# Performance work log

Measured on AMD Instinct MI355X. Metric: run time of the kernel, lower is better.

The kernel has to match this reference:

```python
import jax, jax.numpy as jnp
import numpy as np

VF = 3          # vote_factor
GRID = 0.1      # grid_size
P = 4           # padded per-group capacity (stands in for data-dependent max group size)
RATIO_MAX = 5   # original drops groups needing repeat ratio > 5
EPS = 1e-5
SHIFT, BASE = 512, 1024  # 3D->1D hash (int32-safe: BASE**3 < 2**31)


def _bn_relu(x, gamma, beta):
    # BatchNorm1d in train mode over the token (batch) axis; conv input is (N, C, 1)
    m = x.mean(axis=0)
    v = jnp.mean((x - m) ** 2, axis=0)  # biased variance, as torch BN uses for normalization
    return jax.nn.relu((x - m) * jax.lax.rsqrt(v + EPS) * gamma + beta)


def _one_sample(idv, cov, ftv, W1, b1, g1, be1, W2, b2, g2, be2, W3, b3):
    N, C = ftv.shape
    V = N * VF
    # conv1x1 stack == per-token linear layers
    h = _bn_relu(ftv @ W1.T + b1, g1, be1)
    h = _bn_relu(h @ W2.T + b2, g2, be2)
    log = (h @ W3.T + b3).reshape(N, VF, 3 + C)
    off3 = log[:, :, :3]                                  # (N, VF, 3)
    coor = (cov[:, None, :] + off3).reshape(V, 3)
    grid_res = (off3 / GRID).astype(jnp.int32)            # trunc toward zero, like .int()
    ind = (idv[:, None, :] + grid_res).reshape(V, 3)
    # Degenerate inner-dict loop (tensor keys hash by identity): every vote's feature
    # offset becomes offset[n][VF-1] * 3 / VF  (len(key)==3, idx stale at VF-1)
    feat_off = log[:, VF - 1, 3:] * (3.0 / VF)            # (N, C)
    feat = jnp.broadcast_to((ftv + feat_off)[:, None, :], (N, VF, C)).reshape(V, C)

    # group votes by quantized 3D index (tuple-key dict -> hash + unique + segment ops)
    hc = jnp.clip(ind, -SHIFT, SHIFT - 1) + SHIFT
    keys = (hc[:, 0] * BASE + hc[:, 1]) * BASE + hc[:, 2]  # (V,) int32
    _, inv = jnp.unique(keys, size=V, fill_value=-1, return_inverse=True)
    inv = inv.reshape(-1)
    ones = jnp.ones((V,), jnp.int32)
    counts = jax.ops.segment_sum(ones, inv, num_segments=V)          # group sizes
    order = jnp.argsort(inv)                                          # votes sorted by group
    starts = jnp.cumsum(counts) - counts
    first = jax.ops.segment_min(jnp.arange(V, dtype=jnp.int32), inv, num_segments=V)
    first = jnp.where(counts > 0, first, 0)
    ind_buf = jnp.where((counts > 0)[:, None], ind[first], 0).astype(jnp.int32)

    cnt_safe = jnp.maximum(counts, 1)
    p = jnp.arange(P, dtype=jnp.int32)
    src_pos = starts[:, None] + (p[None, :] % cnt_safe[:, None])      # (V, P) repeat-fill
    src = order[src_pos]
    valid = (counts > 0) & (counts * RATIO_MAX >= P)                  # ceil(P/cnt) <= 5
    coor_buf = jnp.where(valid[:, None, None], coor[src], 0.0)        # (V, P, 3)
    feat_buf = jnp.where(valid[:, None, None], feat[src], 0.0)        # (V, P, C)
    return ind_buf, coor_buf, feat_buf, valid


def setup_inputs() -> dict:
    key = jax.random.key(0)
    ks = jax.random.split(key, 12)
    B, N, C = 2, 16384, 128
    s = 1.0 / np.sqrt(C)
    return {
        "ID": jax.random.randint(ks[0], (B, N, 3), 0, 100, dtype=jnp.int32),
        "CO": jax.random.normal(ks[1], (B, N, 3), jnp.float32),
        "FT": jax.random.normal(ks[2], (B, N, C), jnp.float32),
        "W1": jax.random.normal(ks[3], (C, C), jnp.float32) * s,
        "b1": jnp.zeros((C,), jnp.float32),
        "g1": 1.0 + 0.1 * jax.random.normal(ks[4], (C,), jnp.float32),
        "be1": 0.1 * jax.random.normal(ks[5], (C,), jnp.float32),
        "W2": jax.random.normal(ks[6], (C, C), jnp.float32) * s,
        "b2": jnp.zeros((C,), jnp.float32),
        "g2": 1.0 + 0.1 * jax.random.normal(ks[7], (C,), jnp.float32),
        "be2": 0.1 * jax.random.normal(ks[8], (C,), jnp.float32),
        "W3": jax.random.normal(ks[9], ((3 + C) * VF, C), jnp.float32) * s,
        "b3": 0.01 * jax.random.normal(ks[10], ((3 + C) * VF,), jnp.float32),
    }


def reference(ID, CO, FT, W1, b1, g1, be1, W2, b2, g2, be2, W3, b3):
    outs = [_one_sample(ID[i], CO[i], FT[i], W1, b1, g1, be1, W2, b2, g2, be2, W3, b3)
            for i in range(ID.shape[0])]  # small fixed batch loop
    ind_buf = jnp.stack([o[0] for o in outs])
    coor_buf = jnp.stack([o[1] for o in outs])
    feat_buf = jnp.stack([o[2] for o in outs])
    mask = jnp.stack([o[3] for o in outs])
    return ind_buf, coor_buf, feat_buf, mask
```

## Files before the change

### kernel.cpp

```cpp
#include <hip/hip_runtime.h>

constexpr int Bn = 2;
constexpr int Nn = 16384;
constexpr int Cc = 128;
constexpr int Vv = Nn * 3;
constexpr int Pp = 4;
constexpr int SB = 48;
constexpr int HB = 96;

constexpr size_t IND0  = 0;
constexpr size_t COOR0 = (size_t)Bn * Vv * 3;
constexpr size_t FEAT0 = COOR0 + (size_t)Bn * Vv * Pp * 3;
constexpr size_t MASK0 = FEAT0 + (size_t)Bn * Vv * Pp * Cc;

template<bool BNF, bool ZERO>
__global__ __launch_bounds__(256) void gemm_t(
    const float* __restrict__ A, const float* __restrict__ W,
    const float* __restrict__ bias, const float* __restrict__ part,
    const float* __restrict__ g, const float* __restrict__ be,
    float* __restrict__ out, unsigned* __restrict__ HZ)
{
    __shared__ float As[64 * 36];
    __shared__ float Ws[128 * 36];
    __shared__ float ssl[2 * Cc];

    int t = threadIdx.x;
    if constexpr (ZERO) {
        int gid = blockIdx.x * 256 + t;
        if (gid < 3 * Bn * SB * 1024 / 4)
            ((uint4*)HZ)[gid] = make_uint4(0u, 0u, 0u, 0u);
    }

    int bid = blockIdx.x;
    int s = bid >> 8, rb = bid & 255;
    const float* Ag = A + (size_t)s * Nn * Cc + (size_t)rb * 64 * Cc;
    float* outg = out + (size_t)s * Nn * Cc + (size_t)rb * 64 * Cc;

    if constexpr (BNF) {
        if (t < Cc) {
            const float* pp = part + (size_t)s * 64 * 2 * Cc;
            float sm = 0.f, sq = 0.f;
            for (int b = 0; b < 64; ++b) {
                sm += pp[(size_t)b * 2 * Cc + t];
                sq += pp[(size_t)b * 2 * Cc + Cc + t];
            }
            float m   = sm / (float)Nn;
            float var = sq / (float)Nn - m * m;
            float inv = 1.0f / sqrtf(var + 1e-5f);
            float sc  = g[t] * inv;
            ssl[t]      = sc;
            ssl[Cc + t] = be[t] - m * sc;
        }
        __syncthreads();
    }

    int tx = t & 15, ty = t >> 4;
    int arow = t >> 3, ac4 = (t & 7) * 4;
    int wrow0 = t >> 3;

    float acc[4][8];
    #pragma unroll
    for (int i = 0; i < 4; ++i)
        #pragma unroll
        for (int j = 0; j < 8; ++j) acc[i][j] = 0.f;

    float4 aR[2], wR[4];
    #pragma unroll
    for (int r = 0; r < 2; ++r)
        aR[r] = *(const float4*)(Ag + (size_t)(arow + r * 32) * Cc + ac4);
    #pragma unroll
    for (int r = 0; r < 4; ++r)
        wR[r] = *(const float4*)(W + (size_t)(wrow0 + r * 32) * Cc + ac4);

    for (int stage = 0; stage < 4; ++stage) {
        if (stage) __syncthreads();
        #pragma unroll
        for (int r = 0; r < 2; ++r) {
            float4 v = aR[r];
            if constexpr (BNF) {
                int ch = ac4;
                v.x = fmaxf(0.f, fmaf(v.x, ssl[ch + 0], ssl[Cc + ch + 0]));
                v.y = fmaxf(0.f, fmaf(v.y, ssl[ch + 1], ssl[Cc + ch + 1]));
                v.z = fmaxf(0.f, fmaf(v.z, ssl[ch + 2], ssl[Cc + ch + 2]));
                v.w = fmaxf(0.f, fmaf(v.w, ssl[ch + 3], ssl[Cc + ch + 3]));
            }
            *(float4*)&As[(arow + r * 32) * 36 + ac4] = v;
        }
        #pragma unroll
        for (int r = 0; r < 4; ++r)
            *(float4*)&Ws[(wrow0 + r * 32) * 36 + ac4] = wR[r];
        if (stage < 3) {
            int k1 = (stage + 1) * 32;
            #pragma unroll
            for (int r = 0; r < 2; ++r)
                aR[r] = *(const float4*)(Ag + (size_t)(arow + r * 32) * Cc + k1 + ac4);
            #pragma unroll
            for (int r = 0; r < 4; ++r)
                wR[r] = *(const float4*)(W + (size_t)(wrow0 + r * 32) * Cc + k1 + ac4);
        }
        __syncthreads();
        #pragma unroll
        for (int k4 = 0; k4 < 8; ++k4) {
            int k = k4 * 4;
            float4 av[4];
            #pragma unroll
            for (int i = 0; i < 4; ++i) av[i] = *(const float4*)&As[(i * 16 + ty) * 36 + k];
            #pragma unroll
            for (int j = 0; j < 8; ++j) {
                float4 wv = *(const float4*)&Ws[(j * 16 + tx) * 36 + k];
                #pragma unroll
                for (int i = 0; i < 4; ++i) {
                    float a0 = acc[i][j];
                    a0 = fmaf(av[i].x, wv.x, a0);
                    a0 = fmaf(av[i].y, wv.y, a0);
                    a0 = fmaf(av[i].z, wv.z, a0);
                    a0 = fmaf(av[i].w, wv.w, a0);
                    acc[i][j] = a0;
                }
            }
        }
    }

    #pragma unroll
    for (int j = 0; j < 8; ++j) {
        int col = j * 16 + tx;
        float bv = bias[col];
        #pragma unroll
        for (int i = 0; i < 4; ++i)
            outg[(size_t)(i * 16 + ty) * Cc + col] = acc[i][j] + bv;
    }
}


template<bool ZERO>
__global__ __launch_bounds__(256) void gemm_t2(
    const float* __restrict__ A, const float* __restrict__ W,
    const float* __restrict__ bias, const float* __restrict__ part,
    const float* __restrict__ g, const float* __restrict__ be,
    float* __restrict__ out, unsigned* __restrict__ HZ)
{
    __shared__ float As[64 * 36];
    __shared__ float Ws[128 * 36];
    __shared__ float ssl[2 * Cc];

    int t = threadIdx.x;
    if constexpr (ZERO) {
        int gid = blockIdx.x * 256 + t;
        if (gid < 3 * Bn * SB * 1024 / 4)
            ((uint4*)HZ)[gid] = make_uint4(0u, 0u, 0u, 0u);
    }

    int bid = blockIdx.x;
    int s = bid >> 8, rb = bid & 255;
    const float* Ag = A + (size_t)s * Nn * Cc + (size_t)rb * 64 * Cc;
    float* outg = out + (size_t)s * Nn * Cc + (size_t)rb * 64 * Cc;

    if (t < Cc) {
        const float* pp = part + (size_t)s * 64 * 2 * Cc;
        float sm = 0.f, sq = 0.f;
        for (int b = 0; b < 64; ++b) {
            sm += pp[(size_t)b * 2 * Cc + t];
            sq += pp[(size_t)b * 2 * Cc + Cc + t];
        }
        float m   = sm / (float)Nn;
        float var = sq / (float)Nn - m * m;
        float inv = 1.0f / sqrtf(var + 1e-5f);
        float sc  = g[t] * inv;
        ssl[t]      = sc;
        ssl[Cc + t] = be[t] - m * sc;
    }
    __syncthreads();

    int tx = t & 15, ty = t >> 4;
    int arow = t >> 3, ac4 = (t & 7) * 4;

    float acc[4][8];
    #pragma unroll
    for (int i = 0; i < 4; ++i)
        #pragma unroll
        for (int j = 0; j < 8; ++j) acc[i][j] = 0.f;

    float4 aR[2], wR[4];
    #pragma unroll
    for (int r = 0; r < 2; ++r)
        aR[r] = *(const float4*)(Ag + (size_t)(arow + r * 32) * Cc + ac4);
    #pragma unroll
    for (int r = 0; r < 4; ++r)
        wR[r] = *(const float4*)(W + (size_t)(arow + r * 32) * Cc + ac4);

    for (int stage = 0; stage < 4; ++stage) {
        int k0 = stage * 32;
        if (stage) __syncthreads();
        #pragma unroll
        for (int r = 0; r < 2; ++r) {
            float4 v = aR[r];
            int ch = k0 + ac4;
            v.x = fmaxf(0.f, fmaf(v.x, ssl[ch + 0], ssl[Cc + ch + 0]));
            v.y = fmaxf(0.f, fmaf(v.y, ssl[ch + 1], ssl[Cc + ch + 1]));
            v.z = fmaxf(0.f, fmaf(v.z, ssl[ch + 2], ssl[Cc + ch + 2]));
            v.w = fmaxf(0.f, fmaf(v.w, ssl[ch + 3], ssl[Cc + ch + 3]));
            *(float4*)&As[(arow + r * 32) * 36 + ac4] = v;
        }
        #pragma unroll
        for (int r = 0; r < 4; ++r)
            *(float4*)&Ws[(arow + r * 32) * 36 + ac4] = wR[r];
        if (stage < 3) {
            int k1 = k0 + 32;
            #pragma unroll
            for (int r = 0; r < 2; ++r)
                aR[r] = *(const float4*)(Ag + (size_t)(arow + r * 32) * Cc + k1 + ac4);
            #pragma unroll
            for (int r = 0; r < 4; ++r)
                wR[r] = *(const float4*)(W + (size_t)(arow + r * 32) * Cc + k1 + ac4);
        }
        __syncthreads();
        #pragma unroll
        for (int k4 = 0; k4 < 8; ++k4) {
            int k = k4 * 4;
            float4 av[4];
            #pragma unroll
            for (int i = 0; i < 4; ++i) av[i] = *(const float4*)&As[(i * 16 + ty) * 36 + k];
            #pragma unroll
            for (int j = 0; j < 8; ++j) {
                float4 wv = *(const float4*)&Ws[(j * 16 + tx) * 36 + k];
                #pragma unroll
                for (int i = 0; i < 4; ++i) {
                    float a0 = acc[i][j];
                    a0 = fmaf(av[i].x, wv.x, a0);
                    a0 = fmaf(av[i].y, wv.y, a0);
                    a0 = fmaf(av[i].z, wv.z, a0);
                    a0 = fmaf(av[i].w, wv.w, a0);
                    acc[i][j] = a0;
                }
            }
        }
    }
    #pragma unroll
    for (int j = 0; j < 8; ++j) {
        int col = j * 16 + tx;
        float bv = bias[col];
        #pragma unroll
        for (int i = 0; i < 4; ++i)
            outg[(size_t)(i * 16 + ty) * Cc + col] = acc[i][j] + bv;
    }
}

__global__ __launch_bounds__(256) void gemm3_fused(
    const float* __restrict__ A, const float* __restrict__ W,
    const float* __restrict__ bias, const float* __restrict__ part,
    const float* __restrict__ g, const float* __restrict__ be,
    const float* __restrict__ FT, const float* __restrict__ CO,
    const int* __restrict__ ID,
    float* __restrict__ featb, float* __restrict__ coor,
    int* __restrict__ indb, unsigned* __restrict__ keys,
    unsigned* __restrict__ idx0, unsigned* __restrict__ hist0)
{
    __shared__ float As[64 * 36];
    __shared__ float Ws[144 * 36];
    __shared__ float ssl[2 * Cc];

    int bid = blockIdx.x;
    int s = bid >> 8, rb = bid & 255;
    const float* Ag = A + (size_t)s * Nn * Cc + (size_t)rb * 64 * Cc;

    int t = threadIdx.x, tx = t & 15, ty = t >> 4;

    if (t < Cc) {
        const float* pp = part + (size_t)s * 64 * 2 * Cc;
        float sm = 0.f, sq = 0.f;
        for (int b = 0; b < 64; ++b) {
            sm += pp[(size_t)b * 2 * Cc + t];
            sq += pp[(size_t)b * 2 * Cc + Cc + t];
        }
        float m   = sm / (float)Nn;
        float var = sq / (float)Nn - m * m;
        float inv = 1.0f / sqrtf(var + 1e-5f);
        float sc  = g[t] * inv;
        ssl[t]      = sc;
        ssl[Cc + t] = be[t] - m * sc;
    }
    __syncthreads();

    float acc[4][9];
    #pragma unroll
    for (int i = 0; i < 4; ++i)
        #pragma unroll
        for (int j = 0; j < 9; ++j) acc[i][j] = 0.f;

    for (int stage = 0; stage < 4; ++stage) {
        int k0 = stage * 32;
        if (stage) __syncthreads();
        #pragma unroll
        for (int r = 0; r < 2; ++r) {
            int idx = r * 256 + t;
            int row = idx >> 3, c4 = (idx & 7) * 4;
            float4 v = *(const float4*)(Ag + (size_t)row * Cc + k0 + c4);
            int ch = k0 + c4;
            v.x = fmaxf(0.f, fmaf(v.x, ssl[ch + 0], ssl[Cc + ch + 0]));
            v.y = fmaxf(0.f, fmaf(v.y, ssl[ch + 1], ssl[Cc + ch + 1]));
            v.z = fmaxf(0.f, fmaf(v.z, ssl[ch + 2], ssl[Cc + ch + 2]));
            v.w = fmaxf(0.f, fmaf(v.w, ssl[ch + 3], ssl[Cc + ch + 3]));
            *(float4*)&As[row * 36 + c4] = v;
        }
        for (int idx = t; idx < 144 * 8; idx += 256) {
            int row = idx >> 3, c4 = (idx & 7) * 4;
            float4 v = make_float4(0.f, 0.f, 0.f, 0.f);
            if (row < 137) {
                int wr = (row < 9) ? (row / 3) * 131 + (row % 3) : row + 256;
                v = *(const float4*)(W + (size_t)wr * Cc + k0 + c4);
            }
            *(float4*)&Ws[row * 36 + c4] = v;
        }
        __syncthreads();
        #pragma unroll
        for (int k4 = 0; k4 < 8; ++k4) {
            int k = k4 * 4;
            float4 av[4];
            #pragma unroll
            for (int i = 0; i < 4; ++i) av[i] = *(const float4*)&As[(i * 16 + ty) * 36 + k];
            #pragma unroll
            for (int j = 0; j < 9; ++j) {
                float4 wv = *(const float4*)&Ws[(j * 16 + tx) * 36 + k];
                #pragma unroll
                for (int i = 0; i < 4; ++i) {
                    float a0 = acc[i][j];
                    a0 = fmaf(av[i].x, wv.x, a0);
                    a0 = fmaf(av[i].y, wv.y, a0);
                    a0 = fmaf(av[i].z, wv.z, a0);
                    a0 = fmaf(av[i].w, wv.w, a0);
                    acc[i][j] = a0;
                }
            }
        }
    }

    __syncthreads();
    __shared__ float L9[64 * 12];
    int n0 = rb * 64;
    const float* FTg = FT + ((size_t)s * Nn + n0) * Cc;
    float* FBg = featb + ((size_t)s * Nn + n0) * Cc;
    #pragma unroll
    for (int j = 0; j < 9; ++j) {
        int col = j * 16 + tx;
        if (col < 9) {
            float bv = bias[(col / 3) * 131 + col % 3];
            #pragma unroll
            for (int i = 0; i < 4; ++i)
                L9[(i * 16 + ty) * 12 + col] = acc[i][j] + bv;
        } else if (col < 137) {
            int ch = col - 9;
            float bv = bias[col + 256];
            #pragma unroll
            for (int i = 0; i < 4; ++i) {
                int row = i * 16 + ty;
                float lg = acc[i][j] + bv;
                FBg[(size_t)row * Cc + ch] = FTg[(size_t)row * Cc + ch] + lg;
            }
        }
    }
    __syncthreads();
    if (t < 192) {
        int row = t / 3, jv = t - row * 3;
        int n = n0 + row, v = n * 3 + jv;
        size_t vb = (size_t)s * Vv + v;
        float o0 = L9[row * 12 + jv * 3 + 0];
        float o1 = L9[row * 12 + jv * 3 + 1];
        float o2 = L9[row * 12 + jv * 3 + 2];
        const float* co = CO + ((size_t)s * Nn + n) * 3;
        coor[vb * 3 + 0] = co[0] + o0;
        coor[vb * 3 + 1] = co[1] + o1;
        coor[vb * 3 + 2] = co[2] + o2;
        const int* id = ID + ((size_t)s * Nn + n) * 3;
        int gi0 = (int)(o0 / 0.1f), gi1 = (int)(o1 / 0.1f), gi2 = (int)(o2 / 0.1f);
        int i0 = id[0] + gi0, i1 = id[1] + gi1, i2 = id[2] + gi2;
        indb[vb * 3 + 0] = i0; indb[vb * 3 + 1] = i1; indb[vb * 3 + 2] = i2;
        int h0 = min(max(i0, -512), 511) + 512;
        int h1 = min(max(i1, -512), 511) + 512;
        int h2 = min(max(i2, -512), 511) + 512;
        unsigned key = ((unsigned)h0 * 1024u + (unsigned)h1) * 1024u + (unsigned)h2;
        keys[vb] = key;
        idx0[vb] = (unsigned)v;
        atomicAdd(&hist0[(size_t)s * SB * 1024 + (size_t)(v >> 10) * 1024 + (key & 1023u)], 1u);
    }
}

__global__ void colstats(const float* __restrict__ Y, float* __restrict__ part)
{
    int blk = blockIdx.x;
    int s = blk >> 6, b = blk & 63;
    const float* Yp = Y + (size_t)s * Nn * Cc + (size_t)b * 256 * Cc;
    int c = threadIdx.x;
    float sm = 0.f, sq = 0.f;
    for (int r = 0; r < 256; ++r) {
        float v = Yp[(size_t)r * Cc + c];
        sm += v; sq += v * v;
    }
    float* pp = part + ((size_t)s * 64 + b) * 2 * Cc;
    pp[c] = sm;
    pp[Cc + c] = sq;
}

template<int PASS>
__global__ __launch_bounds__(512) void scat(
    const unsigned* __restrict__ kIn, const unsigned* __restrict__ iIn,
    unsigned* __restrict__ kOut, unsigned* __restrict__ iOut,
    const unsigned* __restrict__ hist, unsigned* __restrict__ nextH)
{
    __shared__ unsigned hw[8 * 1024];
    __shared__ unsigned tot[1024];
    int t = threadIdx.x, lane = t & 63, w = t >> 6;
    int blk = blockIdx.x, s = blk / SB, b = blk % SB;

    #pragma unroll
    for (int i = 0; i < 16; ++i) hw[w * 1024 + i * 64 + lane] = 0u;

    const uint2* hs2 = (const uint2*)(hist + (size_t)s * SB * 1024);
    int d0 = 2 * t, d1 = 2 * t + 1;
    unsigned run0 = 0, run1 = 0, my0 = 0, my1 = 0;
    for (int bb = 0; bb < SB; ++bb) {
        uint2 v = hs2[bb * 512 + t];
        if (bb == b) { my0 = run0; my1 = run1; }
        run0 += v.x; run1 += v.y;
    }
    tot[d0] = run0; tot[d1] = run1;
    __syncthreads();
    for (int ofs = 1; ofs < 1024; ofs <<= 1) {
        unsigned a0 = (d0 >= ofs) ? tot[d0 - ofs] : 0u;
        unsigned a1 = (d1 >= ofs) ? tot[d1 - ofs] : 0u;
        __syncthreads();
        tot[d0] += a0; tot[d1] += a1;
        __syncthreads();
    }
    tot[d0] = tot[d0] - run0 + my0;
    tot[d1] = tot[d1] - run1 + my1;

    size_t base = (size_t)s * Vv + (size_t)b * 1024;
    unsigned keyE[2], idxE[2], rkE[2], dE[2];
    #pragma unroll
    for (int e = 0; e < 2; ++e) {
        int pos = w * 128 + e * 64 + lane;
        keyE[e] = kIn[base + pos];
        idxE[e] = iIn[base + pos];
        unsigned d = (keyE[e] >> (PASS * 10)) & 1023u;
        dE[e] = d;
        unsigned long long m = ~0ull;
        #pragma unroll
        for (int bit = 0; bit < 10; ++bit) {
            bool bbit = (d >> bit) & 1u;
            unsigned long long bal = __ballot(bbit);
            m &= bbit ? bal : ~bal;
        }
        int lanesBelow = __popcll(m & ((1ull << lane) - 1ull));
        int cnt = __popcll(m);
        int leader = __ffsll((unsigned long long)m) - 1;
        unsigned basec = hw[w * 1024 + d];
        if (lane == leader) hw[w * 1024 + d] = basec + (unsigned)cnt;
        rkE[e] = basec + (unsigned)lanesBelow;
    }
    __syncthreads();
    {
        unsigned r0 = 0, r1 = 0;
        for (int ww = 0; ww < 8; ++ww) {
            unsigned v0 = hw[ww * 1024 + d0], v1 = hw[ww * 1024 + d1];
            hw[ww * 1024 + d0] = r0; hw[ww * 1024 + d1] = r1;
            r0 += v0; r1 += v1;
        }
    }
    __syncthreads();
    #pragma unroll
    for (int e = 0; e < 2; ++e) {
        unsigned dest = tot[dE[e]] + hw[w * 1024 + dE[e]] + rkE[e];
        kOut[(size_t)s * Vv + dest] = keyE[e];
        iOut[(size_t)s * Vv + dest] = idxE[e];
        if constexpr (PASS < 2) {
            unsigned d2 = (keyE[e] >> ((PASS + 1) * 10)) & 1023u;
            atomicAdd(&nextH[(size_t)s * SB * 1024 + (size_t)(dest >> 10) * 1024 + d2], 1u);
        }
    }
}

__global__ __launch_bounds__(512) void headsct(const unsigned* __restrict__ skeys,
                                               unsigned* __restrict__ hpart)
{
    int blk = blockIdx.x;
    int s = blk / HB, b = blk % HB;
    int i = b * 512 + threadIdx.x;
    size_t base = (size_t)s * Vv;
    unsigned k = skeys[base + i];
    bool head = (i == 0) || (skeys[base + i - 1] != k);
    __shared__ unsigned wsum[8];
    unsigned long long bal = __ballot(head);
    int lane = threadIdx.x & 63, wid = threadIdx.x >> 6;
    if (lane == 0) wsum[wid] = (unsigned)__popcll(bal);
    __syncthreads();
    if (threadIdx.x == 0) {
        unsigned tot = 0;
        for (int w = 0; w < 8; ++w) tot += wsum[w];
        hpart[s * HB + b] = tot;
    }
}

__global__ __launch_bounds__(512) void ranksk(const unsigned* __restrict__ skeys,
                                              const unsigned* __restrict__ hpart,
                                              unsigned* __restrict__ start,
                                              unsigned* __restrict__ nu)
{
    int blk = blockIdx.x;
    int s = blk / HB, b = blk % HB;
    int t = threadIdx.x;
    __shared__ unsigned hp[HB];
    __shared__ unsigned pre[HB + 1];
    if (t < HB) hp[t] = hpart[s * HB + t];
    __syncthreads();
    if (t == 0) {
        unsigned run = 0;
        for (int i = 0; i < HB; ++i) { pre[i] = run; run += hp[i]; }
        pre[HB] = run;
    }
    __syncthreads();
    int i = b * 512 + t;
    size_t base = (size_t)s * Vv;
    unsigned k = skeys[base + i];
    bool head = (i == 0) || (skeys[base + i - 1] != k);
    unsigned long long bal = __ballot(head);
    int lane = t & 63, wid = t >> 6;
    __shared__ unsigned wsum[8];
    if (lane == 0) wsum[wid] = (unsigned)__popcll(bal);
    __syncthreads();
    unsigned wbase = 0;
    for (int w = 0; w < wid; ++w) wbase += wsum[w];
    unsigned lpre = (unsigned)__popcll(bal & ((1ull << lane) - 1ull));
    if (head)
        start[(size_t)s * (Vv + 1) + pre[b] + wbase + lpre] = (unsigned)i;
    if (b == 0 && t == 0) {
        nu[s] = pre[HB];
        start[(size_t)s * (Vv + 1) + pre[HB]] = (unsigned)Vv;
    }
}

__global__ __launch_bounds__(256) void outputk(
    const unsigned* __restrict__ sidx, const unsigned* __restrict__ start,
    const unsigned* __restrict__ nu, const int* __restrict__ indb,
    const float* __restrict__ coor, const float* __restrict__ featb,
    float* __restrict__ out)
{
    int wid = threadIdx.x >> 6, lane = threadIdx.x & 63;
    int g = blockIdx.x * 4 + wid;
    int s = g / Vv, u = g - s * Vv;
    size_t su = (size_t)s * Vv + u;
    bool valid = (unsigned)u < nu[s];
    float4* out4 = (float4*)out;
    int f = lane & 31, jlo = lane >> 5;
    if (valid) {
        const unsigned* st = start + (size_t)s * (Vv + 1);
        unsigned i0 = st[u], i1 = st[u + 1];
        unsigned c = i1 - i0;
        unsigned my = sidx[(size_t)s * Vv + i0 + ((unsigned)(lane & 3)) % c];
        unsigned sv[4];
        sv[0] = __shfl(my, 0); sv[1] = __shfl(my, 1);
        sv[2] = __shfl(my, 2); sv[3] = __shfl(my, 3);
        const float4* fb = (const float4*)(featb + (size_t)s * Nn * Cc);
        #pragma unroll
        for (int h = 0; h < 2; ++h) {
            int j = jlo + 2 * h;
            out4[(FEAT0 >> 2) + su * 128 + (size_t)j * 32 + f] =
                fb[(size_t)(sv[j] / 3) * 32 + f];
        }
        if (lane < 12)
            out[COOR0 + su * 12 + lane] =
                coor[((size_t)s * Vv + sv[lane / 3]) * 3 + lane % 3];
        else if (lane < 15)
            out[IND0 + su * 3 + (lane - 12)] =
                (float)indb[((size_t)s * Vv + sv[0]) * 3 + (lane - 12)];
        else if (lane == 15)
            out[MASK0 + su] = 1.f;
    } else {
        float4 z = make_float4(0.f, 0.f, 0.f, 0.f);
        #pragma unroll
        for (int h = 0; h < 2; ++h)
            out4[(FEAT0 >> 2) + su * 128 + (size_t)(jlo + 2 * h) * 32 + f] = z;
        if (lane < 12)       out[COOR0 + su * 12 + lane] = 0.f;
        else if (lane < 15)  out[IND0 + su * 3 + (lane - 12)] = 0.f;
        else if (lane == 15) out[MASK0 + su] = 0.f;
    }
}

extern "C" void kernel_launch(void* const* d_in, const int* in_sizes, int n_in,
                              void* d_out, int out_size, void* d_ws, size_t ws_size,
                              hipStream_t stream)
{
    const int*   ID  = (const int*)d_in[0];
    const float* CO  = (const float*)d_in[1];
    const float* FT  = (const float*)d_in[2];
    const float* W1  = (const float*)d_in[3];
    const float* b1  = (const float*)d_in[4];
    const float* g1  = (const float*)d_in[5];
    const float* be1 = (const float*)d_in[6];
    const float* W2  = (const float*)d_in[7];
    const float* b2  = (const float*)d_in[8];
    const float* g2  = (const float*)d_in[9];
    const float* be2 = (const float*)d_in[10];
    const float* W3  = (const float*)d_in[11];
    const float* b3  = (const float*)d_in[12];
    float* out = (float*)d_out;

    char* wsc = (char*)d_ws;
    size_t off = 0;
    auto alloc = [&](size_t elems) -> void* {
        void* p = wsc + off;
        off += ((elems * 4 + 255) & ~(size_t)255);
        return p;
    };
    float*    H1b   = (float*)alloc((size_t)Bn * Nn * Cc);
    float*    H2b   = (float*)alloc((size_t)Bn * Nn * Cc);
    float*    PART  = (float*)alloc((size_t)Bn * 64 * 2 * Cc);
    float*    COORb = (float*)alloc((size_t)Bn * Vv * 3);
    int*      INDB  = (int*)alloc((size_t)Bn * Vv * 3);
    float*    FEATB = (float*)alloc((size_t)Bn * Nn * Cc);
    unsigned* KA    = (unsigned*)alloc((size_t)Bn * Vv);
    unsigned* IA    = (unsigned*)alloc((size_t)Bn * Vv);
    unsigned* KB    = (unsigned*)alloc((size_t)Bn * Vv);
    unsigned* IB    = (unsigned*)alloc((size_t)Bn * Vv);
    unsigned* H0h   = (unsigned*)alloc((size_t)Bn * SB * 1024);
    unsigned* H1h   = (unsigned*)alloc((size_t)Bn * SB * 1024);
    unsigned* H2h   = (unsigned*)alloc((size_t)Bn * SB * 1024);
    unsigned* HP    = (unsigned*)alloc((size_t)Bn * HB);
    unsigned* NUp   = (unsigned*)alloc((size_t)Bn);
    unsigned* STp   = (unsigned*)alloc((size_t)Bn * (Vv + 1));
    (void)in_sizes; (void)n_in; (void)out_size; (void)ws_size;

    gemm_t<false, true><<<Bn * 256, 256, 0, stream>>>(
        FT, W1, b1, nullptr, nullptr, nullptr, H1b, H0h);
    colstats<<<Bn * 64, 128, 0, stream>>>(H1b, PART);
    gemm_t2<false><<<Bn * 256, 256, 0, stream>>>(
        H1b, W2, b2, PART, g1, be1, H2b, nullptr);
    colstats<<<Bn * 64, 128, 0, stream>>>(H2b, PART);
    gemm3_fused<<<Bn * 256, 256, 0, stream>>>(
        H2b, W3, b3, PART, g2, be2, FT, CO, ID, FEATB, COORb, INDB, KA, IA, H0h);
    scat<0><<<Bn * SB, 512, 0, stream>>>(KA, IA, KB, IB, H0h, H1h);
    scat<1><<<Bn * SB, 512, 0, stream>>>(KB, IB, KA, IA, H1h, H2h);
    scat<2><<<Bn * SB, 512, 0, stream>>>(KA, IA, KB, IB, H2h, nullptr);
    headsct<<<Bn * HB, 512, 0, stream>>>(KB, HP);
    ranksk<<<Bn * HB, 512, 0, stream>>>(KB, HP, STp, NUp);
    outputk<<<Bn * Vv / 4, 256, 0, stream>>>(IB, STp, NUp, INDB, COORb, FEATB, out);
}
```

Measured before the change: 214.2 us.

## Merge head-count into rank kernel, wave-scan digit offsets, widen output blocks

The separate head-count kernel is removed. Each rank block now recomputes all per-chunk head counts itself, saving a launch at the cost of redundant reads of the sorted keys. In the radix scatter, the shared-memory Hillis-Steele scan over 1024 digits is replaced by a wavefront shuffle scan plus per-wave totals, which cuts many barriers. The output kernel moves to 512-thread blocks, a few loops get unroll pragmas, and the first GEMM template is simplified.

New measurement: 228.7 us. +6.8%, slower.

```diff
diff --git a/kernel.cpp b/kernel.cpp
--- a/kernel.cpp
+++ b/kernel.cpp
@@ -13,19 +13,16 @@
 constexpr size_t FEAT0 = COOR0 + (size_t)Bn * Vv * Pp * 3;
 constexpr size_t MASK0 = FEAT0 + (size_t)Bn * Vv * Pp * Cc;
 
-template<bool BNF, bool ZERO>
-__global__ __launch_bounds__(256) void gemm_t(
+__global__ __launch_bounds__(256) void gemm1(
     const float* __restrict__ A, const float* __restrict__ W,
-    const float* __restrict__ bias, const float* __restrict__ part,
-    const float* __restrict__ g, const float* __restrict__ be,
-    float* __restrict__ out, unsigned* __restrict__ HZ)
+    const float* __restrict__ bias, float* __restrict__ out,
+    unsigned* __restrict__ HZ)
 {
     __shared__ float As[64 * 36];
     __shared__ float Ws[128 * 36];
-    __shared__ float ssl[2 * Cc];
 
     int t = threadIdx.x;
-    if constexpr (ZERO) {
+    {
         int gid = blockIdx.x * 256 + t;
         if (gid < 3 * Bn * SB * 1024 / 4)
             ((uint4*)HZ)[gid] = make_uint4(0u, 0u, 0u, 0u);
@@ -36,27 +33,8 @@
     const float* Ag = A + (size_t)s * Nn * Cc + (size_t)rb * 64 * Cc;
     float* outg = out + (size_t)s * Nn * Cc + (size_t)rb * 64 * Cc;
 
-    if constexpr (BNF) {
-        if (t < Cc) {
-            const float* pp = part + (size_t)s * 64 * 2 * Cc;
-            float sm = 0.f, sq = 0.f;
-            for (int b = 0; b < 64; ++b) {
-                sm += pp[(size_t)b * 2 * Cc + t];
-                sq += pp[(size_t)b * 2 * Cc + Cc + t];
-            }
-            float m   = sm / (float)Nn;
-            float var = sq / (float)Nn - m * m;
-            float inv = 1.0f / sqrtf(var + 1e-5f);
-            float sc  = g[t] * inv;
-            ssl[t]      = sc;
-            ssl[Cc + t] = be[t] - m * sc;
-        }
-        __syncthreads();
-    }
-
     int tx = t & 15, ty = t >> 4;
     int arow = t >> 3, ac4 = (t & 7) * 4;
-    int wrow0 = t >> 3;
 
     float acc[4][8];
     #pragma unroll
@@ -70,25 +48,16 @@
         aR[r] = *(const float4*)(Ag + (size_t)(arow + r * 32) * Cc + ac4);
     #pragma unroll
     for (int r = 0; r < 4; ++r)
-        wR[r] = *(const float4*)(W + (size_t)(wrow0 + r * 32) * Cc + ac4);
+        wR[r] = *(const float4*)(W + (size_t)(arow + r * 32) * Cc + ac4);
 
     for (int stage = 0; stage < 4; ++stage) {
         if (stage) __syncthreads();
         #pragma unroll
-        for (int r = 0; r < 2; ++r) {
-            float4 v = aR[r];
-            if constexpr (BNF) {
-                int ch = ac4;
-                v.x = fmaxf(0.f, fmaf(v.x, ssl[ch + 0], ssl[Cc + ch + 0]));
-                v.y = fmaxf(0.f, fmaf(v.y, ssl[ch + 1], ssl[Cc + ch + 1]));
-                v.z = fmaxf(0.f, fmaf(v.z, ssl[ch + 2], ssl[Cc + ch + 2]));
-                v.w = fmaxf(0.f, fmaf(v.w, ssl[ch + 3], ssl[Cc + ch + 3]));
-            }
-            *(float4*)&As[(arow + r * 32) * 36 + ac4] = v;
-        }
+        for (int r = 0; r < 2; ++r)
+            *(float4*)&As[(arow + r * 32) * 36 + ac4] = aR[r];
         #pragma unroll
         for (int r = 0; r < 4; ++r)
-            *(float4*)&Ws[(wrow0 + r * 32) * 36 + ac4] = wR[r];
+            *(float4*)&Ws[(arow + r * 32) * 36 + ac4] = wR[r];
         if (stage < 3) {
             int k1 = (stage + 1) * 32;
             #pragma unroll
@@ -96,7 +65,7 @@
                 aR[r] = *(const float4*)(Ag + (size_t)(arow + r * 32) * Cc + k1 + ac4);
             #pragma unroll
             for (int r = 0; r < 4; ++r)
-                wR[r] = *(const float4*)(W + (size_t)(wrow0 + r * 32) * Cc + k1 + ac4);
+                wR[r] = *(const float4*)(W + (size_t)(arow + r * 32) * Cc + k1 + ac4);
         }
         __syncthreads();
         #pragma unroll
@@ -120,7 +89,6 @@
             }
         }
     }
-
     #pragma unroll
     for (int j = 0; j < 8; ++j) {
         int col = j * 16 + tx;
@@ -131,25 +99,17 @@
     }
 }
 
-
-template<bool ZERO>
 __global__ __launch_bounds__(256) void gemm_t2(
     const float* __restrict__ A, const float* __restrict__ W,
     const float* __restrict__ bias, const float* __restrict__ part,
     const float* __restrict__ g, const float* __restrict__ be,
-    float* __restrict__ out, unsigned* __restrict__ HZ)
+    float* __restrict__ out)
 {
     __shared__ float As[64 * 36];
     __shared__ float Ws[128 * 36];
     __shared__ float ssl[2 * Cc];
 
     int t = threadIdx.x;
-    if constexpr (ZERO) {
-        int gid = blockIdx.x * 256 + t;
-        if (gid < 3 * Bn * SB * 1024 / 4)
-            ((uint4*)HZ)[gid] = make_uint4(0u, 0u, 0u, 0u);
-    }
-
     int bid = blockIdx.x;
     int s = bid >> 8, rb = bid & 255;
     const float* Ag = A + (size_t)s * Nn * Cc + (size_t)rb * 64 * Cc;
@@ -158,6 +118,7 @@
     if (t < Cc) {
         const float* pp = part + (size_t)s * 64 * 2 * Cc;
         float sm = 0.f, sq = 0.f;
+        #pragma unroll 8
         for (int b = 0; b < 64; ++b) {
             sm += pp[(size_t)b * 2 * Cc + t];
             sq += pp[(size_t)b * 2 * Cc + Cc + t];
@@ -268,6 +229,7 @@
     if (t < Cc) {
         const float* pp = part + (size_t)s * 64 * 2 * Cc;
         float sm = 0.f, sq = 0.f;
+        #pragma unroll 8
         for (int b = 0; b < 64; ++b) {
             sm += pp[(size_t)b * 2 * Cc + t];
             sq += pp[(size_t)b * 2 * Cc + Cc + t];
@@ -391,6 +353,7 @@
     const float* Yp = Y + (size_t)s * Nn * Cc + (size_t)b * 256 * Cc;
     int c = threadIdx.x;
     float sm = 0.f, sq = 0.f;
+    #pragma unroll 8
     for (int r = 0; r < 256; ++r) {
         float v = Yp[(size_t)r * Cc + c];
         sm += v; sq += v * v;
@@ -408,6 +371,7 @@
 {
     __shared__ unsigned hw[8 * 1024];
     __shared__ unsigned tot[1024];
+    __shared__ unsigned wtot[8];
     int t = threadIdx.x, lane = t & 63, w = t >> 6;
     int blk = blockIdx.x, s = blk / SB, b = blk % SB;
 
@@ -417,22 +381,30 @@
     const uint2* hs2 = (const uint2*)(hist + (size_t)s * SB * 1024);
     int d0 = 2 * t, d1 = 2 * t + 1;
     unsigned run0 = 0, run1 = 0, my0 = 0, my1 = 0;
+    #pragma unroll 4
     for (int bb = 0; bb < SB; ++bb) {
         uint2 v = hs2[bb * 512 + t];
         if (bb == b) { my0 = run0; my1 = run1; }
         run0 += v.x; run1 += v.y;
     }
-    tot[d0] = run0; tot[d1] = run1;
-    __syncthreads();
-    for (int ofs = 1; ofs < 1024; ofs <<= 1) {
-        unsigned a0 = (d0 >= ofs) ? tot[d0 - ofs] : 0u;
-        unsigned a1 = (d1 >= ofs) ? tot[d1 - ofs] : 0u;
-        __syncthreads();
-        tot[d0] += a0; tot[d1] += a1;
-        __syncthreads();
-    }
-    tot[d0] = tot[d0] - run0 + my0;
-    tot[d1] = tot[d1] - run1 + my1;
+    unsigned pair = run0 + run1;
+    unsigned S = pair;
+    #pragma unroll
+    for (int o = 1; o < 64; o <<= 1) {
+        unsigned v = __shfl_up(S, o);
+        if (lane >= o) S += v;
+    }
+    unsigned pairExcl = S - pair;
+    unsigned wTot = __shfl(S, 63);
+    if (lane == 63) wtot[w] = S;
+    __syncthreads();
+    unsigned waveBase = 0;
+    #pragma unroll
+    for (int ww = 0; ww < 8; ++ww)
+        if (ww < w) waveBase += wtot[ww];
+    (void)wTot;
+    tot[d0] = waveBase + pairExcl + my0;
+    tot[d1] = waveBase + pairExcl + run0 + my1;
 
     size_t base = (size_t)s * Vv + (size_t)b * 1024;
     unsigned keyE[2], idxE[2], rkE[2], dE[2];
@@ -479,73 +451,63 @@
     }
 }
 
-__global__ __launch_bounds__(512) void headsct(const unsigned* __restrict__ skeys,
-                                               unsigned* __restrict__ hpart)
+__global__ __launch_bounds__(512) void ranksall(const unsigned* __restrict__ skeys,
+                                                unsigned* __restrict__ start,
+                                                unsigned* __restrict__ nu)
 {
     int blk = blockIdx.x;
-    int s = blk / HB, b = blk % HB;
-    int i = b * 512 + threadIdx.x;
+    int s = blk / HB, cb = blk % HB;
+    int t = threadIdx.x, lane = t & 63, w = t >> 6;
     size_t base = (size_t)s * Vv;
-    unsigned k = skeys[base + i];
-    bool head = (i == 0) || (skeys[base + i - 1] != k);
+
+    __shared__ unsigned cnt[HB];
+    __shared__ unsigned pre[HB + 1];
     __shared__ unsigned wsum[8];
-    unsigned long long bal = __ballot(head);
-    int lane = threadIdx.x & 63, wid = threadIdx.x >> 6;
-    if (lane == 0) wsum[wid] = (unsigned)__popcll(bal);
-    __syncthreads();
-    if (threadIdx.x == 0) {
-        unsigned tot = 0;
-        for (int w = 0; w < 8; ++w) tot += wsum[w];
-        hpart[s * HB + b] = tot;
-    }
-}
-
-__global__ __launch_bounds__(512) void ranksk(const unsigned* __restrict__ skeys,
-                                              const unsigned* __restrict__ hpart,
-                                              unsigned* __restrict__ start,
-                                              unsigned* __restrict__ nu)
-{
-    int blk = blockIdx.x;
-    int s = blk / HB, b = blk % HB;
-    int t = threadIdx.x;
-    __shared__ unsigned hp[HB];
-    __shared__ unsigned pre[HB + 1];
-    if (t < HB) hp[t] = hpart[s * HB + t];
+
+    for (int cc = w * 12; cc < w * 12 + 12; ++cc) {
+        unsigned tc = 0;
+        #pragma unroll
+        for (int sub = 0; sub < 8; ++sub) {
+            int i = cc * 512 + sub * 64 + lane;
+            unsigned k = skeys[base + i];
+            bool head = (i == 0) || (skeys[base + i - 1] != k);
+            tc += (unsigned)__popcll(__ballot(head));
+        }
+        if (lane == 0) cnt[cc] = tc;
+    }
     __syncthreads();
     if (t == 0) {
         unsigned run = 0;
-        for (int i = 0; i < HB; ++i) { pre[i] = run; run += hp[i]; }
+        for (int i = 0; i < HB; ++i) { pre[i] = run; run += cnt[i]; }
         pre[HB] = run;
     }
     __syncthreads();
-    int i = b * 512 + t;
-    size_t base = (size_t)s * Vv;
+
+    int i = cb * 512 + t;
     unsigned k = skeys[base + i];
     bool head = (i == 0) || (skeys[base + i - 1] != k);
     unsigned long long bal = __ballot(head);
-    int lane = t & 63, wid = t >> 6;
-    __shared__ unsigned wsum[8];
-    if (lane == 0) wsum[wid] = (unsigned)__popcll(bal);
+    if (lane == 0) wsum[w] = (unsigned)__popcll(bal);
     __syncthreads();
     unsigned wbase = 0;
-    for (int w = 0; w < wid; ++w) wbase += wsum[w];
+    for (int ww = 0; ww < w; ++ww) wbase += wsum[ww];
     unsigned lpre = (unsigned)__popcll(bal & ((1ull << lane) - 1ull));
     if (head)
-        start[(size_t)s * (Vv + 1) + pre[b] + wbase + lpre] = (unsigned)i;
-    if (b == 0 && t == 0) {
+        start[(size_t)s * (Vv + 1) + pre[cb] + wbase + lpre] = (unsigned)i;
+    if (cb == 0 && t == 0) {
         nu[s] = pre[HB];
         start[(size_t)s * (Vv + 1) + pre[HB]] = (unsigned)Vv;
     }
 }
 
-__global__ __launch_bounds__(256) void outputk(
+__global__ __launch_bounds__(512) void outputk(
     const unsigned* __restrict__ sidx, const unsigned* __restrict__ start,
     const unsigned* __restrict__ nu, const int* __restrict__ indb,
     const float* __restrict__ coor, const float* __restrict__ featb,
     float* __restrict__ out)
 {
     int wid = threadIdx.x >> 6, lane = threadIdx.x & 63;
-    int g = blockIdx.x * 4 + wid;
+    int g = blockIdx.x * 8 + wid;
     int s = g / Vv, u = g - s * Vv;
     size_t su = (size_t)s * Vv + u;
     bool valid = (unsigned)u < nu[s];
@@ -624,23 +586,19 @@
     unsigned* H0h   = (unsigned*)alloc((size_t)Bn * SB * 1024);
     unsigned* H1h   = (unsigned*)alloc((size_t)Bn * SB * 1024);
     unsigned* H2h   = (unsigned*)alloc((size_t)Bn * SB * 1024);
-    unsigned* HP    = (unsigned*)alloc((size_t)Bn * HB);
     unsigned* NUp   = (unsigned*)alloc((size_t)Bn);
     unsigned* STp   = (unsigned*)alloc((size_t)Bn * (Vv + 1));
     (void)in_sizes; (void)n_in; (void)out_size; (void)ws_size;
 
-    gemm_t<false, true><<<Bn * 256, 256, 0, stream>>>(
-        FT, W1, b1, nullptr, nullptr, nullptr, H1b, H0h);
+    gemm1<<<Bn * 256, 256, 0, stream>>>(FT, W1, b1, H1b, H0h);
     colstats<<<Bn * 64, 128, 0, stream>>>(H1b, PART);
-    gemm_t2<false><<<Bn * 256, 256, 0, stream>>>(
-        H1b, W2, b2, PART, g1, be1, H2b, nullptr);
+    gemm_t2<<<Bn * 256, 256, 0, stream>>>(H1b, W2, b2, PART, g1, be1, H2b);
     colstats<<<Bn * 64, 128, 0, stream>>>(H2b, PART);
     gemm3_fused<<<Bn * 256, 256, 0, stream>>>(
         H2b, W3, b3, PART, g2, be2, FT, CO, ID, FEATB, COORb, INDB, KA, IA, H0h);
     scat<0><<<Bn * SB, 512, 0, stream>>>(KA, IA, KB, IB, H0h, H1h);
     scat<1><<<Bn * SB, 512, 0, stream>>>(KB, IB, KA, IA, H1h, H2h);
     scat<2><<<Bn * SB, 512, 0, stream>>>(KA, IA, KB, IB, H2h, nullptr);
-    headsct<<<Bn * HB, 512, 0, stream>>>(KB, HP);
-    ranksk<<<Bn * HB, 512, 0, stream>>>(KB, HP, STp, NUp);
-    outputk<<<Bn * Vv / 4, 256, 0, stream>>>(IB, STp, NUp, INDB, COORb, FEATB, out);
-}
+    ranksall<<<Bn * HB, 512, 0, stream>>>(KB, STp, NUp);
+    outputk<<<Bn * Vv / 8, 512, 0, stream>>>(IB, STp, NUp, INDB, COORb, FEATB, out);
+}
```
